# Performance work log

Hardware: AMD Instinct MI355X
Metric: run time of the kernel (lower is better)

Reference implementation:

```python
import jax, jax.numpy as jnp
import numpy as np

B, N, C = 16, 8192, 384   # batch, points, feature dim
G, M = 512, 32            # num_group (FPS centers), group_size (KNN k)


def setup_inputs() -> dict:
    key = jax.random.key(0)
    k1, k2 = jax.random.split(key)
    xyz = jax.random.normal(k1, (B, N, 3), dtype=jnp.float32)
    features = jax.random.normal(k2, (B, N, C), dtype=jnp.float32)
    return {"xyz": xyz, "features": features}


def _fps(xyz, n_samples):
    """Farthest point sampling, deterministic start at index 0 (matches CUDA op).
    xyz: [B, N, 3] -> idx: [B, n_samples] int32."""
    b, n, _ = xyz.shape
    big = jnp.asarray(1e10, xyz.dtype)

    def step(carry, _):
        min_dist, farthest = carry
        centroid = jnp.take_along_axis(xyz, farthest[:, None, None], axis=1)  # [B,1,3]
        d = jnp.sum((xyz - centroid) ** 2, axis=-1)                            # [B,N]
        min_dist = jnp.minimum(min_dist, d)
        nxt = jnp.argmax(min_dist, axis=-1).astype(jnp.int32)
        return (min_dist, nxt), farthest

    init = (jnp.full((b, n), big, xyz.dtype), jnp.zeros((b,), jnp.int32))
    _, idxs = jax.lax.scan(step, init, None, length=n_samples)  # [G, B]
    return jnp.transpose(idxs)  # [B, G]


def _knn_idx(ref, query, k):
    """Indices of k nearest ref points for each query. ref [B,N,3], query [B,G,3] -> [B,G,k]."""
    d = (jnp.sum(query ** 2, -1)[..., None]
         + jnp.sum(ref ** 2, -1)[:, None, :]
         - 2.0 * jnp.einsum('bgd,bnd->bgn', query, ref))  # [B,G,N]
    _, idx = jax.lax.top_k(-d, k)
    return idx


def reference(xyz, features):
    fps_idx = _fps(xyz, G)                                        # [B,G]
    center = jnp.take_along_axis(xyz, fps_idx[..., None], axis=1)  # [B,G,3]
    idx = _knn_idx(xyz, center, M)                                 # [B,G,M]

    gather = jax.vmap(lambda pts, i: pts[i])                       # per-batch fancy gather
    flat_idx = idx.reshape(B, G * M)
    neighborhood = gather(xyz, flat_idx).reshape(B, G, M, 3)
    feature_group = gather(features, flat_idx).reshape(B, G, M, C)
    neighborhood = neighborhood - center[:, :, None, :]
    return neighborhood, center, feature_group
```

## Files before the change

### kernel.cpp

```cpp
#include <hip/hip_runtime.h>
#include <math.h>

#define BATCH 16
#define NPTS  8192
#define FEATC 384
#define NG    512
#define KM    32

#define OUT0_OFF 0
#define OUT1_OFF (BATCH * NG * KM * 3)
#define OUT2_OFF (OUT1_OFF + BATCH * NG * 3)

#pragma clang fp contract(off)

typedef float f32x2 __attribute__((ext_vector_type(2)));

template <int CTRL>
__device__ __forceinline__ unsigned long long dpp_u64(unsigned long long k) {
    unsigned lo = (unsigned)k, hi = (unsigned)(k >> 32);
    lo = (unsigned)__builtin_amdgcn_update_dpp((int)lo, (int)lo, CTRL, 0xF, 0xF, false);
    hi = (unsigned)__builtin_amdgcn_update_dpp((int)hi, (int)hi, CTRL, 0xF, 0xF, false);
    return ((unsigned long long)hi << 32) | lo;
}

__device__ __forceinline__ unsigned long long wave_max_u64(unsigned long long k) {
    unsigned long long o;
    o = dpp_u64<0x111>(k); if (o > k) k = o;
    o = dpp_u64<0x112>(k); if (o > k) k = o;
    o = dpp_u64<0x114>(k); if (o > k) k = o;
    o = dpp_u64<0x118>(k); if (o > k) k = o;
    o = dpp_u64<0x142>(k); if (o > k) k = o;
    o = dpp_u64<0x143>(k); if (o > k) k = o;
    return k;
}

__device__ __forceinline__ unsigned long long wave_min_u64(unsigned long long k) {
    unsigned long long o;
    o = dpp_u64<0x111>(k); if (o < k) k = o;
    o = dpp_u64<0x112>(k); if (o < k) k = o;
    o = dpp_u64<0x114>(k); if (o < k) k = o;
    o = dpp_u64<0x118>(k); if (o < k) k = o;
    o = dpp_u64<0x142>(k); if (o < k) k = o;
    o = dpp_u64<0x143>(k); if (o < k) k = o;
    return k;
}

__device__ __forceinline__ unsigned long long min16_u64(const unsigned long long* k) {
    unsigned long long t8[8];
#pragma unroll
    for (int i = 0; i < 8; ++i) t8[i] = k[i] < k[i + 8] ? k[i] : k[i + 8];
    unsigned long long t4[4];
#pragma unroll
    for (int i = 0; i < 4; ++i) t4[i] = t8[i] < t8[i + 4] ? t8[i] : t8[i + 4];
    unsigned long long a = t4[0] < t4[2] ? t4[0] : t4[2];
    unsigned long long b = t4[1] < t4[3] ? t4[1] : t4[3];
    return a < b ? a : b;
}

__global__ void init_progress(int* progress) {
    if (threadIdx.x < BATCH)
        __hip_atomic_store(&progress[threadIdx.x], 0,
                           __ATOMIC_RELAXED, __HIP_MEMORY_SCOPE_AGENT);
}

__global__ __launch_bounds__(512) void group_kernel(const float* __restrict__ xyz,
                                                    const float* __restrict__ features,
                                                    float* __restrict__ out0,
                                                    float* __restrict__ out1,
                                                    float* __restrict__ out2,
                                                    int* __restrict__ progress) {
#pragma clang fp contract(off)
    __shared__ unsigned long long sk[2][8];
    __shared__ int   sidx[KM];
    __shared__ float sc[3];

    const int tid  = threadIdx.x;
    const int lane = tid & 63;
    const int wid  = tid >> 6;

    if (blockIdx.x < BATCH) {
        const int b = blockIdx.x;
        const float* xb = xyz + (size_t)b * NPTS * 3;
        unsigned* co = (unsigned*)out1 + (size_t)b * NG * 3;

        f32x2 X[8], Y[8], Z[8], MD[8];
#pragma unroll
        for (int j = 0; j < 8; ++j) {
            int p0 = tid + 1024 * j;
            int p1 = p0 + 512;
            X[j]  = (f32x2){xb[p0 * 3 + 0], xb[p1 * 3 + 0]};
            Y[j]  = (f32x2){xb[p0 * 3 + 1], xb[p1 * 3 + 1]};
            Z[j]  = (f32x2){xb[p0 * 3 + 2], xb[p1 * 3 + 2]};
            MD[j] = (f32x2){1e10f, 1e10f};
        }

        int far = 0;
        for (int g = 0; g < NG; ++g) {
            const float cx = xb[far * 3 + 0];
            const float cy = xb[far * 3 + 1];
            const float cz = xb[far * 3 + 2];
            if (tid == 0) {
                __hip_atomic_store(co + g * 3 + 0, __float_as_uint(cx),
                                   __ATOMIC_RELAXED, __HIP_MEMORY_SCOPE_AGENT);
                __hip_atomic_store(co + g * 3 + 1, __float_as_uint(cy),
                                   __ATOMIC_RELAXED, __HIP_MEMORY_SCOPE_AGENT);
                __hip_atomic_store(co + g * 3 + 2, __float_as_uint(cz),
                                   __ATOMIC_RELAXED, __HIP_MEMORY_SCOPE_AGENT);
            }
            const f32x2 cx2 = (f32x2){cx, cx};
            const f32x2 cy2 = (f32x2){cy, cy};
            const f32x2 cz2 = (f32x2){cz, cz};

#pragma unroll
            for (int j = 0; j < 8; ++j) {
                f32x2 dx = X[j] - cx2;
                f32x2 dy = Y[j] - cy2;
                f32x2 dz = Z[j] - cz2;
                f32x2 d  = (dx * dx + dy * dy) + dz * dz;
                MD[j] = __builtin_elementwise_min(MD[j], d);
            }
            f32x2 a0 = __builtin_elementwise_max(MD[0], MD[1]);
            f32x2 a1 = __builtin_elementwise_max(MD[2], MD[3]);
            f32x2 a2 = __builtin_elementwise_max(MD[4], MD[5]);
            f32x2 a3 = __builtin_elementwise_max(MD[6], MD[7]);
            f32x2 b0 = __builtin_elementwise_max(a0, a1);
            f32x2 b1 = __builtin_elementwise_max(a2, a3);
            f32x2 c0 = __builtin_elementwise_max(b0, b1);
            float lmax = fmaxf(c0.x, c0.y);

            unsigned candX = 0xFFFFFFFFu, candY = 0xFFFFFFFFu;
#pragma unroll
            for (int j = 7; j >= 0; --j) {
                if (MD[j].y == lmax) candY = (unsigned)(tid + 1024 * j + 512);
                if (MD[j].x == lmax) candX = (unsigned)(tid + 1024 * j);
            }
            unsigned cand = candX < candY ? candX : candY;

            unsigned long long key =
                ((unsigned long long)__float_as_uint(lmax) << 32) | (unsigned)(~cand);
            key = wave_max_u64(key);

            const int par = g & 1;
            if (lane == 63) sk[par][wid] = key;
            __syncthreads();

            unsigned long long m0 = sk[par][0] > sk[par][1] ? sk[par][0] : sk[par][1];
            unsigned long long m1 = sk[par][2] > sk[par][3] ? sk[par][2] : sk[par][3];
            unsigned long long m2 = sk[par][4] > sk[par][5] ? sk[par][4] : sk[par][5];
            unsigned long long m3 = sk[par][6] > sk[par][7] ? sk[par][6] : sk[par][7];
            unsigned long long ma = m0 > m1 ? m0 : m1;
            unsigned long long mb = m2 > m3 ? m2 : m3;
            unsigned long long gk = ma > mb ? ma : mb;
            far = (int)(~(unsigned)gk);

            if (tid == 0 && (g & 7) == 7)
                __hip_atomic_store(&progress[b], g + 1,
                                   __ATOMIC_RELEASE, __HIP_MEMORY_SCOPE_AGENT);
        }
        return;
    }

    const int i = blockIdx.x - BATCH;
    const int b = i & 15;
    const int g = i >> 4;
    const int bgrow = b * NG + g;

    if (tid == 0) {
        while ((int)__hip_atomic_load(&progress[b], __ATOMIC_ACQUIRE,
                                      __HIP_MEMORY_SCOPE_AGENT) < g + 1)
            __builtin_amdgcn_s_sleep(32);
        unsigned* co = (unsigned*)out1 + (size_t)bgrow * 3;
        sc[0] = __uint_as_float(__hip_atomic_load(co + 0, __ATOMIC_RELAXED,
                                                  __HIP_MEMORY_SCOPE_AGENT));
        sc[1] = __uint_as_float(__hip_atomic_load(co + 1, __ATOMIC_RELAXED,
                                                  __HIP_MEMORY_SCOPE_AGENT));
        sc[2] = __uint_as_float(__hip_atomic_load(co + 2, __ATOMIC_RELAXED,
                                                  __HIP_MEMORY_SCOPE_AGENT));
    }
    __syncthreads();

    const float cx = sc[0], cy = sc[1], cz = sc[2];
    const float q2 = (cx * cx + cy * cy) + cz * cz;

    const float* xb = xyz + (size_t)b * NPTS * 3;

    unsigned long long k[16];
#pragma unroll
    for (int j = 0; j < 16; ++j) {
        int p = tid + (j << 9);
        float rx = xb[p * 3 + 0];
        float ry = xb[p * 3 + 1];
        float rz = xb[p * 3 + 2];
        float r2 = (rx * rx + ry * ry) + rz * rz;
        float dot = fmaf(cz, rz, fmaf(cy, ry, cx * rx));
        float d = (q2 + r2) - 2.0f * dot;
        unsigned u = __float_as_uint(d);
        u ^= ((unsigned)((int)u >> 31)) | 0x80000000u;
        k[j] = ((unsigned long long)u << 32) | (unsigned)p;
    }

    unsigned long long lv = min16_u64(k);

    for (int kk = 0; kk < KM; ++kk) {
        unsigned long long w = wave_min_u64(lv);
        const int par = kk & 1;
        if (lane == 63) sk[par][wid] = w;
        __syncthreads();
        unsigned long long m0 = sk[par][0] < sk[par][1] ? sk[par][0] : sk[par][1];
        unsigned long long m1 = sk[par][2] < sk[par][3] ? sk[par][2] : sk[par][3];
        unsigned long long m2 = sk[par][4] < sk[par][5] ? sk[par][4] : sk[par][5];
        unsigned long long m3 = sk[par][6] < sk[par][7] ? sk[par][6] : sk[par][7];
        unsigned long long ma = m0 < m1 ? m0 : m1;
        unsigned long long mb = m2 < m3 ? m2 : m3;
        unsigned long long gk = ma < mb ? ma : mb;
        const unsigned pt = (unsigned)gk;
        if ((pt & 511u) == (unsigned)tid) {
            sidx[kk] = (int)pt;
            const unsigned jw = pt >> 9;
#pragma unroll
            for (int j = 0; j < 16; ++j) {
                if ((unsigned)j == jw) k[j] = ~0ULL;
            }
            lv = min16_u64(k);
        }
    }
    __syncthreads();

    if (tid < 96) {
        int m = tid / 3;
        int c = tid - 3 * m;
        int p = sidx[m];
        float v = xb[p * 3 + c] - sc[c];
        out0[((size_t)bgrow * KM + m) * 3 + c] = v;
    }

    const float4* fb = (const float4*)(features + (size_t)b * NPTS * FEATC);
    float4*       ob = (float4*)(out2 + (size_t)bgrow * KM * FEATC);
#pragma unroll
    for (int r = 0; r < 6; ++r) {
        int flat = tid + (r << 9);
        int m  = flat / 96;
        int c4 = flat - 96 * m;
        float4 v = fb[(size_t)sidx[m] * 96 + c4];
        ob[(size_t)m * 96 + c4] = v;
    }
}

extern "C" void kernel_launch(void* const* d_in, const int* in_sizes, int n_in,
                              void* d_out, int out_size, void* d_ws, size_t ws_size,
                              hipStream_t stream) {
    const float* xyz      = (const float*)d_in[0];
    const float* features = (const float*)d_in[1];
    float* out  = (float*)d_out;
    float* out0 = out + OUT0_OFF;
    float* out1 = out + OUT1_OFF;
    float* out2 = out + OUT2_OFF;

    int* progress = (int*)d_ws;

    init_progress<<<1, 64, 0, stream>>>(progress);
    group_kernel<<<BATCH + BATCH * NG, 512, 0, stream>>>(xyz, features,
                                                         out0, out1, out2,
                                                         progress);
}
```

Measured before the change: 700.1 us.

## Batch FPS center stores, raise FPS wave priority, and skip redundant KNN wave reductions

FPS blocks now buffer eight centers in shared memory and write them to global memory in one batch alongside the progress flag, instead of three atomic stores per iteration. FPS blocks also raise their wave priority so the serial sampling chain competes better with the KNN blocks sharing the CU. In the KNN top-k loop, only the wave that owned the selected point redoes its wave-level min reduction; the other waves reuse their cached key. This cuts cross-lane DPP work per iteration at the cost of a slightly more complex control flow.

Measured after the change: 700.8 us. About the same (+0.1%).

```diff
diff --git a/kernel.cpp b/kernel.cpp
--- a/kernel.cpp
+++ b/kernel.cpp
@@ -72,16 +72,17 @@
 #pragma clang fp contract(off)
     __shared__ unsigned long long sk[2][8];
     __shared__ int   sidx[KM];
-    __shared__ float sc[3];
+    __shared__ float scst[24];
 
     const int tid  = threadIdx.x;
     const int lane = tid & 63;
     const int wid  = tid >> 6;
 
     if (blockIdx.x < BATCH) {
+        __builtin_amdgcn_s_setprio(3);
         const int b = blockIdx.x;
         const float* xb = xyz + (size_t)b * NPTS * 3;
-        unsigned* co = (unsigned*)out1 + (size_t)b * NG * 3;
+        float* co = out1 + (size_t)b * NG * 3;
 
         f32x2 X[8], Y[8], Z[8], MD[8];
 #pragma unroll
@@ -100,12 +101,9 @@
             const float cy = xb[far * 3 + 1];
             const float cz = xb[far * 3 + 2];
             if (tid == 0) {
-                __hip_atomic_store(co + g * 3 + 0, __float_as_uint(cx),
-                                   __ATOMIC_RELAXED, __HIP_MEMORY_SCOPE_AGENT);
-                __hip_atomic_store(co + g * 3 + 1, __float_as_uint(cy),
-                                   __ATOMIC_RELAXED, __HIP_MEMORY_SCOPE_AGENT);
-                __hip_atomic_store(co + g * 3 + 2, __float_as_uint(cz),
-                                   __ATOMIC_RELAXED, __HIP_MEMORY_SCOPE_AGENT);
+                scst[(g & 7) * 3 + 0] = cx;
+                scst[(g & 7) * 3 + 1] = cy;
+                scst[(g & 7) * 3 + 2] = cz;
             }
             const f32x2 cx2 = (f32x2){cx, cx};
             const f32x2 cy2 = (f32x2){cy, cy};
@@ -153,9 +151,12 @@
             unsigned long long gk = ma > mb ? ma : mb;
             far = (int)(~(unsigned)gk);
 
-            if (tid == 0 && (g & 7) == 7)
-                __hip_atomic_store(&progress[b], g + 1,
-                                   __ATOMIC_RELEASE, __HIP_MEMORY_SCOPE_AGENT);
+            if ((g & 7) == 7) {
+                if (tid < 24) co[(g - 7) * 3 + tid] = scst[tid];
+                if (tid == 0)
+                    __hip_atomic_store(&progress[b], g + 1,
+                                       __ATOMIC_RELEASE, __HIP_MEMORY_SCOPE_AGENT);
+            }
         }
         return;
     }
@@ -170,16 +171,16 @@
                                       __HIP_MEMORY_SCOPE_AGENT) < g + 1)
             __builtin_amdgcn_s_sleep(32);
         unsigned* co = (unsigned*)out1 + (size_t)bgrow * 3;
-        sc[0] = __uint_as_float(__hip_atomic_load(co + 0, __ATOMIC_RELAXED,
-                                                  __HIP_MEMORY_SCOPE_AGENT));
-        sc[1] = __uint_as_float(__hip_atomic_load(co + 1, __ATOMIC_RELAXED,
-                                                  __HIP_MEMORY_SCOPE_AGENT));
-        sc[2] = __uint_as_float(__hip_atomic_load(co + 2, __ATOMIC_RELAXED,
-                                                  __HIP_MEMORY_SCOPE_AGENT));
+        scst[0] = __uint_as_float(__hip_atomic_load(co + 0, __ATOMIC_RELAXED,
+                                                    __HIP_MEMORY_SCOPE_AGENT));
+        scst[1] = __uint_as_float(__hip_atomic_load(co + 1, __ATOMIC_RELAXED,
+                                                    __HIP_MEMORY_SCOPE_AGENT));
+        scst[2] = __uint_as_float(__hip_atomic_load(co + 2, __ATOMIC_RELAXED,
+                                                    __HIP_MEMORY_SCOPE_AGENT));
     }
     __syncthreads();
 
-    const float cx = sc[0], cy = sc[1], cz = sc[2];
+    const float cx = scst[0], cy = scst[1], cz = scst[2];
     const float q2 = (cx * cx + cy * cy) + cz * cz;
 
     const float* xb = xyz + (size_t)b * NPTS * 3;
@@ -200,12 +201,13 @@
     }
 
     unsigned long long lv = min16_u64(k);
+    unsigned long long wkey = wave_min_u64(lv);
+    if (lane == 63) sk[0][wid] = wkey;
+    __syncthreads();
 
     for (int kk = 0; kk < KM; ++kk) {
-        unsigned long long w = wave_min_u64(lv);
         const int par = kk & 1;
-        if (lane == 63) sk[par][wid] = w;
-        __syncthreads();
+        const int nxt = par ^ 1;
         unsigned long long m0 = sk[par][0] < sk[par][1] ? sk[par][0] : sk[par][1];
         unsigned long long m1 = sk[par][2] < sk[par][3] ? sk[par][2] : sk[par][3];
         unsigned long long m2 = sk[par][4] < sk[par][5] ? sk[par][4] : sk[par][5];
@@ -214,23 +216,31 @@
         unsigned long long mb = m2 < m3 ? m2 : m3;
         unsigned long long gk = ma < mb ? ma : mb;
         const unsigned pt = (unsigned)gk;
-        if ((pt & 511u) == (unsigned)tid) {
-            sidx[kk] = (int)pt;
-            const unsigned jw = pt >> 9;
-#pragma unroll
-            for (int j = 0; j < 16; ++j) {
-                if ((unsigned)j == jw) k[j] = ~0ULL;
-            }
-            lv = min16_u64(k);
+        const int wwave = (int)((pt & 511u) >> 6);
+
+        if (wid == wwave) {
+            if ((pt & 511u) == (unsigned)tid) {
+                sidx[kk] = (int)pt;
+                const unsigned jw = pt >> 9;
+#pragma unroll
+                for (int j = 0; j < 16; ++j) {
+                    if ((unsigned)j == jw) k[j] = ~0ULL;
+                }
+                lv = min16_u64(k);
+            }
+            wkey = wave_min_u64(lv);
+            if (lane == 63) sk[nxt][wid] = wkey;
+        } else {
+            if (lane == 63) sk[nxt][wid] = wkey;
         }
-    }
-    __syncthreads();
+        __syncthreads();
+    }
 
     if (tid < 96) {
         int m = tid / 3;
         int c = tid - 3 * m;
         int p = sidx[m];
-        float v = xb[p * 3 + c] - sc[c];
+        float v = xb[p * 3 + c] - scst[c];
         out0[((size_t)bgrow * KM + m) * 3 + c] = v;
     }
 
```
